# Kernel optimization log

Hardware: AMD Instinct MI355X
Metric: run time of the kernel (lower is better)

## Reference

```python
import jax, jax.numpy as jnp
import numpy as np
import math

D = 256; NH = 8; NL = 1; K = 5; P = K * K; HD = D // NH; DFF = 1024
N = 8192; H = 512; W = 512


def _kernel_indices():
    # odd kernel: linspace(-(K-1)/2, (K-1)/2, K) / K, meshgrid ij, stacked (x=j, y=i)
    idx = jnp.linspace(-(K - 1) / 2, (K - 1) / 2, K)
    i, j = jnp.meshgrid(idx, idx, indexing='ij')
    return jnp.stack([j, i], axis=-1).reshape(-1, 2) / K  # (P, 2)


def _ln(x, g, b, eps=1e-5):
    m = x.mean(-1, keepdims=True)
    v = ((x - m) ** 2).mean(-1, keepdims=True)
    return (x - m) / jnp.sqrt(v + eps) * g + b


def setup_inputs() -> dict:
    key = jax.random.key(0)
    ks = jax.random.split(key, 20)
    s = 0.02
    inp = {
        'query': jax.random.normal(ks[0], (1, N, D), jnp.float32),
        'memory': jax.random.normal(ks[1], (1, H * W, D), jnp.float32),
        'ref_windows': jax.random.uniform(ks[2], (1, N, 8), jnp.float32),
        'memory_shape': jnp.array([[H, W]], jnp.int32),
        'memory_start_idx': jnp.zeros((1,), jnp.int64),
        # pos embed MLP(8 -> D -> D -> D)
        'Wp1': jax.random.normal(ks[3], (D, 8)) * s, 'bp1': jnp.zeros((D,)),
        'Wp2': jax.random.normal(ks[4], (D, D)) * s, 'bp2': jnp.zeros((D,)),
        'Wp3': jax.random.normal(ks[5], (D, D)) * s, 'bp3': jnp.zeros((D,)),
        # Box3dAttention
        'Wv': jax.random.normal(ks[6], (D, D)) * s, 'bv': jnp.zeros((D,)),
        'Wa': jax.random.normal(ks[7], (NH * NL * P, D)) * s, 'ba': jnp.zeros((NH * NL * P,)),
        'Wb': jax.random.normal(ks[8], (NH * NL * 5, D)) * s, 'bb': jnp.zeros((NH * NL * 5,)),
        'Wo': jax.random.normal(ks[9], (D, D)) * s, 'bo': jnp.zeros((D,)),
        # FFN + norms
        'W1': jax.random.normal(ks[10], (DFF, D)) * s, 'b1': jnp.zeros((DFF,)),
        'W2': jax.random.normal(ks[11], (D, DFF)) * s, 'b2': jnp.zeros((D,)),
        'g2': jnp.ones((D,)), 'be2': jnp.zeros((D,)),
        'g3': jnp.ones((D,)), 'be3': jnp.zeros((D,)),
    }
    return inp


def reference(query, memory, ref_windows, memory_shape, memory_start_idx,
              Wp1, bp1, Wp2, bp2, Wp3, bp3, Wv, bv, Wa, ba, Wb, bb, Wo, bo,
              W1, b1, W2, b2, g2, be2, g3, be3):
    B, n, _ = query.shape  # B == 1, single level (NL == 1)
    # query positional embedding from ref windows (3-layer MLP)
    qp = jax.nn.relu(ref_windows @ Wp1.T + bp1)
    qp = jax.nn.relu(qp @ Wp2.T + bp2)
    qp = qp @ Wp3.T + bp3
    q = query + qp

    # --- Box3dAttention ---
    v = (memory @ Wv.T + bv).reshape(B, H * W, NH, HD)
    attn = jax.nn.softmax((q @ Wa.T + ba).reshape(B, n, NH, NL * P), axis=-1)
    attn = attn.reshape(B, n, NH, NL, P)

    off = (q @ Wb.T + bb).reshape(B, n, NH, NL, 5)
    off_box, off_ang = off[..., :4], off[..., 4:]
    rw = ref_windows[:, :, None, None]                     # (B,n,1,1,8)
    ref_boxes = rw[..., jnp.array([0, 1, 3, 4])]           # cx,cy,w,l
    ref_angle = rw[..., 6:7]
    angles = (ref_angle + off_ang / 16.0) * (2.0 * math.pi)  # (B,n,NH,NL,1)
    boxes = ref_boxes + off_box / 8.0 * ref_boxes[..., jnp.array([2, 3, 2, 3])]
    center = boxes[..., None, :2]                          # (B,n,NH,NL,1,2)
    size = jax.nn.relu(boxes[..., None, 2:])
    grid = _kernel_indices() * size                        # (B,n,NH,NL,P,2)
    c, sgn = jnp.cos(angles), jnp.sin(angles)
    rot = jnp.stack([c, -sgn, sgn, c], -1).reshape(B, n, NH, NL, 1, 2, 2)
    loc = center + (grid[..., None, :] * rot).sum(-1)      # (B,n,NH,NL,P,2) in [0,1]

    # bilinear sampling (grid_sample, align_corners=False, zero padding), single level
    loc0 = loc[0, :, :, 0]                                 # (n,NH,P,2)
    vh = v[0].transpose(1, 0, 2)                           # (NH,HW,HD)
    x = loc0[..., 0] * W - 0.5
    y = loc0[..., 1] * H - 0.5
    x0 = jnp.floor(x); y0 = jnp.floor(y)
    hidx = jnp.arange(NH)[None, :, None]
    out = jnp.zeros((n, NH, P, HD), v.dtype)
    for dx, dy in ((0, 0), (1, 0), (0, 1), (1, 1)):
        xi = x0 + dx; yi = y0 + dy
        wgt = (1.0 - jnp.abs(x - xi)) * (1.0 - jnp.abs(y - yi))
        valid = (xi >= 0) & (xi <= W - 1) & (yi >= 0) & (yi <= H - 1)
        idx = (jnp.clip(yi, 0, H - 1) * W + jnp.clip(xi, 0, W - 1)).astype(jnp.int32)
        g = vh[hidx, idx]                                  # (n,NH,P,HD)
        out = out + jnp.where(valid, wgt, 0.0)[..., None] * g
    out = (out * attn[0, :, :, 0, :, None]).sum(2)         # (n,NH,HD)
    q2 = out.reshape(1, n, D) @ Wo.T + bo

    # residual + LN + FFN + LN
    xq = _ln(query + q2, g2, be2)
    ff = jax.nn.relu(xq @ W1.T + b1) @ W2.T + b2
    return _ln(xq + ff, g3, be3)
```

## Files before the change

kernel.cpp:

```cpp
#include <hip/hip_runtime.h>
#include <hip/hip_bf16.h>
#include <math.h>

#define NQ 8192
#define DD 256
#define NHD 8
#define HDD 32
#define PP 25
#define HH 512
#define WW 512
#define HWSZ (HH * WW)
#define DFF 1024

typedef __bf16 bf16_t;
typedef bf16_t bf16x8 __attribute__((ext_vector_type(8)));
typedef bf16_t bf16x4 __attribute__((ext_vector_type(4)));
typedef float f32x4 __attribute__((ext_vector_type(4)));

template <int A_F32, int RELU, int ADD_RES, int BF16_OUT>
__global__ __launch_bounds__(256) void gemm_mfma(
    const void* __restrict__ Av, const bf16_t* __restrict__ Wt,
    const float* __restrict__ bias, const float* __restrict__ res,
    void* __restrict__ Cout, int M, int N, int K) {
  __shared__ bf16_t As[128][32];
  __shared__ bf16_t Bs[128][32];
  const int tid = threadIdx.x;
  const int bn = blockIdx.x * 128;
  const int bm = blockIdx.y * 128;
  const int wave = tid >> 6;
  const int lane = tid & 63;
  const int l15 = lane & 15;
  const int quad = lane >> 4;
  const int wm = (wave & 1) * 64;
  const int wn = (wave >> 1) * 64;

  f32x4 acc[4][4];
#pragma unroll
  for (int i = 0; i < 4; i++)
#pragma unroll
    for (int j = 0; j < 4; j++) acc[i][j] = (f32x4){0.f, 0.f, 0.f, 0.f};

  const int srow = tid >> 2;
  const int skq = (tid & 3) * 8;

  for (int k0 = 0; k0 < K; k0 += 32) {
    if (A_F32) {
      const float* A = (const float*)Av;
#pragma unroll
      for (int c = 0; c < 4; c++) {
        const int id = c * 256 + tid;
        const int row = id >> 3;
        const int kq = (id & 7) * 4;
        const float4 av = *(const float4*)(A + (long)(bm + row) * K + k0 + kq);
        bf16x4 bv;
        bv[0] = (bf16_t)av.x;
        bv[1] = (bf16_t)av.y;
        bv[2] = (bf16_t)av.z;
        bv[3] = (bf16_t)av.w;
        *(bf16x4*)&As[row][kq] = bv;
      }
    } else {
      const bf16_t* A = (const bf16_t*)Av;
#pragma unroll
      for (int c = 0; c < 2; c++) {
        const int row = c * 64 + srow;
        const bf16_t* gp = A + (long)(bm + row) * K + k0 + skq;
        bf16_t* lp = &As[0][0] + (c * 2048 + wave * 512);
        __builtin_amdgcn_global_load_lds(
            (const __attribute__((address_space(1))) void*)gp,
            (__attribute__((address_space(3))) void*)lp, 16, 0, 0);
      }
    }
#pragma unroll
    for (int c = 0; c < 2; c++) {
      const int row = c * 64 + srow;
      int wrow = bn + row;
      if (wrow >= N) wrow = N - 1;
      const bf16_t* gp = Wt + (long)wrow * K + k0 + skq;
      bf16_t* lp = &Bs[0][0] + (c * 2048 + wave * 512);
      __builtin_amdgcn_global_load_lds(
          (const __attribute__((address_space(1))) void*)gp,
          (__attribute__((address_space(3))) void*)lp, 16, 0, 0);
    }
    __syncthreads();
    bf16x8 af[4], bfr[4];
#pragma unroll
    for (int i = 0; i < 4; i++)
      af[i] = *(bf16x8*)&As[wm + i * 16 + l15][quad * 8];
#pragma unroll
    for (int j = 0; j < 4; j++)
      bfr[j] = *(bf16x8*)&Bs[wn + j * 16 + l15][quad * 8];
#pragma unroll
    for (int i = 0; i < 4; i++)
#pragma unroll
      for (int j = 0; j < 4; j++)
        acc[i][j] = __builtin_amdgcn_mfma_f32_16x16x32_bf16(af[i], bfr[j],
                                                            acc[i][j], 0, 0, 0);
    __syncthreads();
  }

  float bsv[4];
#pragma unroll
  for (int j = 0; j < 4; j++) {
    const int n = bn + wn + j * 16 + l15;
    bsv[j] = (n < N) ? bias[n] : 0.f;
  }
#pragma unroll
  for (int i = 0; i < 4; i++) {
#pragma unroll
    for (int r = 0; r < 4; r++) {
      const int m = bm + wm + i * 16 + quad * 4 + r;
#pragma unroll
      for (int j = 0; j < 4; j++) {
        const int n = bn + wn + j * 16 + l15;
        if (n < N) {
          float v = acc[i][j][r] + bsv[j];
          if (ADD_RES) v += res[(long)m * N + n];
          if (RELU) v = fmaxf(v, 0.f);
          if (BF16_OUT)
            ((__hip_bfloat16*)Cout)[(long)m * N + n] = __float2bfloat16(v);
          else
            ((float*)Cout)[(long)m * N + n] = v;
        }
      }
    }
  }
}

struct CastArgs {
  const float* src[8];
  __hip_bfloat16* dst[8];
  int len[8];
};
__global__ __launch_bounds__(256) void cast_weights(CastArgs a) {
  const int seg = blockIdx.y;
  const int base = blockIdx.x * 1024 + threadIdx.x * 4;
  if (base >= a.len[seg]) return;
  const float4 v = *(const float4*)(a.src[seg] + base);
  __hip_bfloat16* d = a.dst[seg] + base;
  d[0] = __float2bfloat16(v.x);
  d[1] = __float2bfloat16(v.y);
  d[2] = __float2bfloat16(v.z);
  d[3] = __float2bfloat16(v.w);
}

__global__ __launch_bounds__(256) void qp1_kernel(
    const float* __restrict__ rw, const float* __restrict__ Wp1,
    const float* __restrict__ bp1, __hip_bfloat16* __restrict__ out) {
  const int m = blockIdx.x;
  const int d = threadIdx.x;
  __shared__ float r[8];
  if (d < 8) r[d] = rw[m * 8 + d];
  __syncthreads();
  float s = bp1[d];
#pragma unroll
  for (int j = 0; j < 8; j++) s += r[j] * Wp1[d * 8 + j];
  out[(long)m * DD + d] = __float2bfloat16(fmaxf(s, 0.f));
}

__global__ __launch_bounds__(256) void attn_loc_kernel(
    const float* __restrict__ logits, const float* __restrict__ offp,
    const float* __restrict__ rw, float* __restrict__ attn,
    float* __restrict__ loc) {
  const int m = blockIdx.x;
  const int t = threadIdx.x;
  __shared__ float sl[200];
  __shared__ float soff[40];
  __shared__ float srw[8];
  if (t < 200) sl[t] = logits[(long)m * 200 + t];
  if (t >= 208 && t < 248) soff[t - 208] = offp[(long)m * 40 + (t - 208)];
  if (t >= 200 && t < 208) srw[t - 200] = rw[(long)m * 8 + (t - 200)];
  __syncthreads();
  if (t < 8) {
    float mx = -1e30f;
    for (int p = 0; p < 25; p++) mx = fmaxf(mx, sl[t * 25 + p]);
    float s = 0.f;
    for (int p = 0; p < 25; p++) s += __expf(sl[t * 25 + p] - mx);
    const float inv = 1.f / s;
    for (int p = 0; p < 25; p++)
      attn[(long)m * 200 + t * 25 + p] = __expf(sl[t * 25 + p] - mx) * inv;
  }
  if (t < 200) {
    const int h = t / 25;
    const int p = t - h * 25;
    const float cx = srw[0], cy = srw[1], w0 = srw[3], h0 = srw[4],
                ra = srw[6];
    const float ob0 = soff[h * 5 + 0], ob1 = soff[h * 5 + 1],
                ob2 = soff[h * 5 + 2], ob3 = soff[h * 5 + 3],
                oa = soff[h * 5 + 4];
    const float ang = (ra + oa * (1.f / 16.f)) * 6.28318530717958647692f;
    const float bx = cx + ob0 * 0.125f * w0;
    const float by = cy + ob1 * 0.125f * h0;
    const float bw = fmaxf(w0 + ob2 * 0.125f * w0, 0.f);
    const float bh = fmaxf(h0 + ob3 * 0.125f * h0, 0.f);
    const float gx = (float)((p % 5) - 2) * 0.2f * bw;
    const float gy = (float)((p / 5) - 2) * 0.2f * bh;
    float sn, cs;
    __sincosf(ang, &sn, &cs);
    loc[((long)m * 200 + t) * 2 + 0] = bx + cs * gx - sn * gy;
    loc[((long)m * 200 + t) * 2 + 1] = by + sn * gx + cs * gy;
  }
}

__global__ __launch_bounds__(256) void sample_kernel(
    const __hip_bfloat16* __restrict__ v, const float* __restrict__ attn,
    const float* __restrict__ loc, __hip_bfloat16* __restrict__ out) {
  const int m = blockIdx.x;
  const int t = threadIdx.x;
  const int h = t >> 5;
  const int c = t & 31;
  __shared__ float sat[200];
  __shared__ float slc[400];
  if (t < 200) sat[t] = attn[(long)m * 200 + t];
  slc[t] = loc[(long)m * 400 + t];
  if (t < 144) slc[256 + t] = loc[(long)m * 400 + 256 + t];
  __syncthreads();
  float acc = 0.f;
  for (int p = 0; p < 25; p++) {
    const float lx = slc[(h * 25 + p) * 2 + 0];
    const float ly = slc[(h * 25 + p) * 2 + 1];
    const float a = sat[h * 25 + p];
    const float x = lx * (float)WW - 0.5f;
    const float y = ly * (float)HH - 0.5f;
    const float x0 = floorf(x);
    const float y0 = floorf(y);
    float sval = 0.f;
#pragma unroll
    for (int dy = 0; dy < 2; dy++)
#pragma unroll
      for (int dx = 0; dx < 2; dx++) {
        const float xi = x0 + (float)dx;
        const float yi = y0 + (float)dy;
        const float wgt = (1.f - fabsf(x - xi)) * (1.f - fabsf(y - yi));
        const bool valid = (xi >= 0.f) && (xi <= (float)(WW - 1)) &&
                           (yi >= 0.f) && (yi <= (float)(HH - 1));
        const int xc = (int)fminf(fmaxf(xi, 0.f), (float)(WW - 1));
        const int yc = (int)fminf(fmaxf(yi, 0.f), (float)(HH - 1));
        const int idx = yc * WW + xc;
        const float g = __bfloat162float(v[(long)idx * DD + h * HDD + c]);
        sval += (valid ? wgt : 0.f) * g;
      }
    acc += a * sval;
  }
  out[(long)m * DD + t] = __float2bfloat16(acc);
}

__global__ __launch_bounds__(256) void ln_kernel(
    const float* __restrict__ x, const float* __restrict__ resid,
    const float* __restrict__ g, const float* __restrict__ b,
    float* __restrict__ out, __hip_bfloat16* __restrict__ out_bf) {
  const int m = blockIdx.x;
  const int d = threadIdx.x;
  const float v = x[(long)m * DD + d] + resid[(long)m * DD + d];
  __shared__ float red[256];
  __shared__ float mean_s, inv_s;
  red[d] = v;
  __syncthreads();
  for (int s = 128; s > 0; s >>= 1) {
    if (d < s) red[d] += red[d + s];
    __syncthreads();
  }
  if (d == 0) mean_s = red[0] * (1.f / 256.f);
  __syncthreads();
  const float mu = mean_s;
  const float diff = v - mu;
  red[d] = diff * diff;
  __syncthreads();
  for (int s = 128; s > 0; s >>= 1) {
    if (d < s) red[d] += red[d + s];
    __syncthreads();
  }
  if (d == 0) inv_s = rsqrtf(red[0] * (1.f / 256.f) + 1e-5f);
  __syncthreads();
  const float o = diff * inv_s * g[d] + b[d];
  out[(long)m * DD + d] = o;
  if (out_bf) out_bf[(long)m * DD + d] = __float2bfloat16(o);
}

extern "C" void kernel_launch(void* const* d_in, const int* in_sizes, int n_in,
                              void* d_out, int out_size, void* d_ws,
                              size_t ws_size, hipStream_t stream) {
  const float* query = (const float*)d_in[0];
  const float* memory = (const float*)d_in[1];
  const float* rw = (const float*)d_in[2];
  const float* Wp1 = (const float*)d_in[5];
  const float* bp1 = (const float*)d_in[6];
  const float* Wp2 = (const float*)d_in[7];
  const float* bp2 = (const float*)d_in[8];
  const float* Wp3 = (const float*)d_in[9];
  const float* bp3 = (const float*)d_in[10];
  const float* Wv = (const float*)d_in[11];
  const float* bv = (const float*)d_in[12];
  const float* Wa = (const float*)d_in[13];
  const float* ba = (const float*)d_in[14];
  const float* Wb = (const float*)d_in[15];
  const float* bb = (const float*)d_in[16];
  const float* Wo = (const float*)d_in[17];
  const float* bo = (const float*)d_in[18];
  const float* W1 = (const float*)d_in[19];
  const float* b1 = (const float*)d_in[20];
  const float* W2 = (const float*)d_in[21];
  const float* b2 = (const float*)d_in[22];
  const float* g2 = (const float*)d_in[23];
  const float* be2 = (const float*)d_in[24];
  const float* g3 = (const float*)d_in[25];
  const float* be3 = (const float*)d_in[26];

  char* ws = (char*)d_ws;
  size_t off = 0;
  auto alloc = [&](size_t bytes) {
    void* p = ws + off;
    off += (bytes + 255) & ~(size_t)255;
    return p;
  };
  __hip_bfloat16* vbuf = (__hip_bfloat16*)alloc((size_t)HWSZ * DD * 2);
  __hip_bfloat16* qp1bf = (__hip_bfloat16*)alloc((size_t)NQ * DD * 2);
  __hip_bfloat16* qp2bf = (__hip_bfloat16*)alloc((size_t)NQ * DD * 2);
  __hip_bfloat16* qbf = (__hip_bfloat16*)alloc((size_t)NQ * DD * 2);
  __hip_bfloat16* oabf = (__hip_bfloat16*)alloc((size_t)NQ * DD * 2);
  __hip_bfloat16* xqbf = (__hip_bfloat16*)alloc((size_t)NQ * DD * 2);
  __hip_bfloat16* h1bf = (__hip_bfloat16*)alloc((size_t)NQ * DFF * 2);
  float* xq32 = (float*)alloc((size_t)NQ * DD * 4);
  float* f32buf = (float*)alloc((size_t)NQ * DD * 4);
  float* offbuf = (float*)alloc((size_t)NQ * 40 * 4);
  float* attnbuf = (float*)alloc((size_t)NQ * 200 * 4);
  float* locbuf = (float*)alloc((size_t)NQ * 200 * 2 * 4);
  __hip_bfloat16* Wp2b = (__hip_bfloat16*)alloc(65536 * 2);
  __hip_bfloat16* Wp3b = (__hip_bfloat16*)alloc(65536 * 2);
  __hip_bfloat16* Wvb = (__hip_bfloat16*)alloc(65536 * 2);
  __hip_bfloat16* Wab = (__hip_bfloat16*)alloc(51200 * 2);
  __hip_bfloat16* Wbb = (__hip_bfloat16*)alloc(10240 * 2);
  __hip_bfloat16* Wob = (__hip_bfloat16*)alloc(65536 * 2);
  __hip_bfloat16* W1b = (__hip_bfloat16*)alloc(262144 * 2);
  __hip_bfloat16* W2b = (__hip_bfloat16*)alloc(262144 * 2);
  (void)ws_size;

  CastArgs ca;
  ca.src[0] = Wp2; ca.dst[0] = Wp2b; ca.len[0] = 65536;
  ca.src[1] = Wp3; ca.dst[1] = Wp3b; ca.len[1] = 65536;
  ca.src[2] = Wv;  ca.dst[2] = Wvb;  ca.len[2] = 65536;
  ca.src[3] = Wa;  ca.dst[3] = Wab;  ca.len[3] = 51200;
  ca.src[4] = Wb;  ca.dst[4] = Wbb;  ca.len[4] = 10240;
  ca.src[5] = Wo;  ca.dst[5] = Wob;  ca.len[5] = 65536;
  ca.src[6] = W1;  ca.dst[6] = W1b;  ca.len[6] = 262144;
  ca.src[7] = W2;  ca.dst[7] = W2b;  ca.len[7] = 262144;
  cast_weights<<<dim3(256, 8), 256, 0, stream>>>(ca);

  qp1_kernel<<<NQ, 256, 0, stream>>>(rw, Wp1, bp1, qp1bf);
  gemm_mfma<0, 1, 0, 1><<<dim3(2, NQ / 128), 256, 0, stream>>>(
      qp1bf, (const bf16_t*)Wp2b, bp2, nullptr, qp2bf, NQ, DD, DD);
  gemm_mfma<0, 0, 1, 1><<<dim3(2, NQ / 128), 256, 0, stream>>>(
      qp2bf, (const bf16_t*)Wp3b, bp3, query, qbf, NQ, DD, DD);
  gemm_mfma<1, 0, 0, 1><<<dim3(2, HWSZ / 128), 256, 0, stream>>>(
      memory, (const bf16_t*)Wvb, bv, nullptr, vbuf, HWSZ, DD, DD);
  gemm_mfma<0, 0, 0, 0><<<dim3(2, NQ / 128), 256, 0, stream>>>(
      qbf, (const bf16_t*)Wab, ba, nullptr, f32buf, NQ, 200, DD);
  gemm_mfma<0, 0, 0, 0><<<dim3(1, NQ / 128), 256, 0, stream>>>(
      qbf, (const bf16_t*)Wbb, bb, nullptr, offbuf, NQ, 40, DD);
  attn_loc_kernel<<<NQ, 256, 0, stream>>>(f32buf, offbuf, rw, attnbuf, locbuf);
  sample_kernel<<<NQ, 256, 0, stream>>>(vbuf, attnbuf, locbuf, oabf);
  gemm_mfma<0, 0, 0, 0><<<dim3(2, NQ / 128), 256, 0, stream>>>(
      oabf, (const bf16_t*)Wob, bo, nullptr, f32buf, NQ, DD, DD);
  ln_kernel<<<NQ, 256, 0, stream>>>(f32buf, query, g2, be2, xq32, xqbf);
  gemm_mfma<0, 1, 0, 1><<<dim3(8, NQ / 128), 256, 0, stream>>>(
      xqbf, (const bf16_t*)W1b, b1, nullptr, h1bf, NQ, DFF, DD);
  gemm_mfma<0, 0, 0, 0><<<dim3(2, NQ / 128), 256, 0, stream>>>(
      h1bf, (const bf16_t*)W2b, b2, nullptr, f32buf, NQ, DD, DFF);
  ln_kernel<<<NQ, 256, 0, stream>>>(f32buf, xq32, g3, be3, (float*)d_out,
                                    nullptr);
}
```

Baseline: 778.1 us.

## Add register-resident-weight value projection kernel and vectorize bilinear sampling taps

Replaces the generic LDS-tiled GEMM for the large memory value projection with a dedicated kernel. Each wave keeps its 64-column slice of Wv in registers and streams fp32 memory rows directly into MFMA fragments, so the weight is never reloaded through shared memory and the A tile skips the LDS round trip. The sampling kernel now assigns one bilinear tap and four channels to each thread, using 8-byte vector loads and cross-lane shuffles to combine the four taps. The trade-offs are higher register pressure in the new projection kernel and extra shuffles in the sampler.

```diff
diff --git a/kernel.cpp b/kernel.cpp
--- a/kernel.cpp
+++ b/kernel.cpp
@@ -17,9 +17,71 @@
 typedef bf16_t bf16x4 __attribute__((ext_vector_type(4)));
 typedef float f32x4 __attribute__((ext_vector_type(4)));
 
-template <int A_F32, int RELU, int ADD_RES, int BF16_OUT>
+__global__ __launch_bounds__(256, 2) void wv_kernel(
+    const float* __restrict__ A, const bf16_t* __restrict__ Wt,
+    const float* __restrict__ bias, __hip_bfloat16* __restrict__ V) {
+  const int tid = threadIdx.x;
+  const int wave = tid >> 6;
+  const int lane = tid & 63;
+  const int l15 = lane & 15;
+  const int quad = lane >> 4;
+  const int wslice = wave * 64;
+  const int base = blockIdx.x * 256;
+
+  bf16x8 bfr[4][8];
+#pragma unroll
+  for (int j = 0; j < 4; j++) {
+    const bf16_t* wp = Wt + (size_t)(wslice + j * 16 + l15) * 256 + quad * 8;
+#pragma unroll
+    for (int kt = 0; kt < 8; kt++) bfr[j][kt] = *(const bf16x8*)(wp + kt * 32);
+  }
+  float bsv[4];
+#pragma unroll
+  for (int j = 0; j < 4; j++) bsv[j] = bias[wslice + j * 16 + l15];
+
+  for (int c = 0; c < 16; c++) {
+    const int m0 = base + c * 16;
+    const float* ap = A + (size_t)(m0 + l15) * 256 + quad * 8;
+    float4 av[8][2];
+#pragma unroll
+    for (int kt = 0; kt < 8; kt++) {
+      av[kt][0] = *(const float4*)(ap + kt * 32);
+      av[kt][1] = *(const float4*)(ap + kt * 32 + 4);
+    }
+    f32x4 acc[4];
+#pragma unroll
+    for (int j = 0; j < 4; j++) acc[j] = (f32x4){0.f, 0.f, 0.f, 0.f};
+#pragma unroll
+    for (int kt = 0; kt < 8; kt++) {
+      bf16x8 afr;
+      afr[0] = (bf16_t)av[kt][0].x;
+      afr[1] = (bf16_t)av[kt][0].y;
+      afr[2] = (bf16_t)av[kt][0].z;
+      afr[3] = (bf16_t)av[kt][0].w;
+      afr[4] = (bf16_t)av[kt][1].x;
+      afr[5] = (bf16_t)av[kt][1].y;
+      afr[6] = (bf16_t)av[kt][1].z;
+      afr[7] = (bf16_t)av[kt][1].w;
+#pragma unroll
+      for (int j = 0; j < 4; j++)
+        acc[j] = __builtin_amdgcn_mfma_f32_16x16x32_bf16(afr, bfr[j][kt],
+                                                         acc[j], 0, 0, 0);
+    }
+#pragma unroll
+    for (int j = 0; j < 4; j++) {
+      const int col = wslice + j * 16 + l15;
+#pragma unroll
+      for (int r = 0; r < 4; r++) {
+        const int row = m0 + quad * 4 + r;
+        V[(size_t)row * DD + col] = __float2bfloat16(acc[j][r] + bsv[j]);
+      }
+    }
+  }
+}
+
+template <int RELU, int ADD_RES, int BF16_OUT>
 __global__ __launch_bounds__(256) void gemm_mfma(
-    const void* __restrict__ Av, const bf16_t* __restrict__ Wt,
+    const bf16_t* __restrict__ A, const bf16_t* __restrict__ Wt,
     const float* __restrict__ bias, const float* __restrict__ res,
     void* __restrict__ Cout, int M, int N, int K) {
   __shared__ bf16_t As[128][32];
@@ -44,32 +106,14 @@
   const int skq = (tid & 3) * 8;
 
   for (int k0 = 0; k0 < K; k0 += 32) {
-    if (A_F32) {
-      const float* A = (const float*)Av;
-#pragma unroll
-      for (int c = 0; c < 4; c++) {
-        const int id = c * 256 + tid;
-        const int row = id >> 3;
-        const int kq = (id & 7) * 4;
-        const float4 av = *(const float4*)(A + (long)(bm + row) * K + k0 + kq);
-        bf16x4 bv;
-        bv[0] = (bf16_t)av.x;
-        bv[1] = (bf16_t)av.y;
-        bv[2] = (bf16_t)av.z;
-        bv[3] = (bf16_t)av.w;
-        *(bf16x4*)&As[row][kq] = bv;
-      }
-    } else {
-      const bf16_t* A = (const bf16_t*)Av;
-#pragma unroll
-      for (int c = 0; c < 2; c++) {
-        const int row = c * 64 + srow;
-        const bf16_t* gp = A + (long)(bm + row) * K + k0 + skq;
-        bf16_t* lp = &As[0][0] + (c * 2048 + wave * 512);
-        __builtin_amdgcn_global_load_lds(
-            (const __attribute__((address_space(1))) void*)gp,
-            (__attribute__((address_space(3))) void*)lp, 16, 0, 0);
-      }
+#pragma unroll
+    for (int c = 0; c < 2; c++) {
+      const int row = c * 64 + srow;
+      const bf16_t* gp = A + (long)(bm + row) * K + k0 + skq;
+      bf16_t* lp = &As[0][0] + (c * 2048 + wave * 512);
+      __builtin_amdgcn_global_load_lds(
+          (const __attribute__((address_space(1))) void*)gp,
+          (__attribute__((address_space(3))) void*)lp, 16, 0, 0);
     }
 #pragma unroll
     for (int c = 0; c < 2; c++) {
@@ -203,46 +247,56 @@
 }
 
 __global__ __launch_bounds__(256) void sample_kernel(
-    const __hip_bfloat16* __restrict__ v, const float* __restrict__ attn,
-    const float* __restrict__ loc, __hip_bfloat16* __restrict__ out) {
+    const bf16_t* __restrict__ v, const float* __restrict__ attn,
+    const float* __restrict__ loc, bf16_t* __restrict__ out) {
   const int m = blockIdx.x;
   const int t = threadIdx.x;
   const int h = t >> 5;
-  const int c = t & 31;
+  const int sub = t & 31;
+  const int tap = sub >> 3;
+  const int ch4 = (sub & 7) * 4;
+  const float fdx = (float)(tap & 1);
+  const float fdy = (float)(tap >> 1);
   __shared__ float sat[200];
   __shared__ float slc[400];
   if (t < 200) sat[t] = attn[(long)m * 200 + t];
   slc[t] = loc[(long)m * 400 + t];
   if (t < 144) slc[256 + t] = loc[(long)m * 400 + 256 + t];
   __syncthreads();
-  float acc = 0.f;
+  float a0 = 0.f, a1 = 0.f, a2 = 0.f, a3 = 0.f;
+  const bf16_t* vb = v + h * HDD + ch4;
   for (int p = 0; p < 25; p++) {
     const float lx = slc[(h * 25 + p) * 2 + 0];
     const float ly = slc[(h * 25 + p) * 2 + 1];
-    const float a = sat[h * 25 + p];
+    const float aw = sat[h * 25 + p];
     const float x = lx * (float)WW - 0.5f;
     const float y = ly * (float)HH - 0.5f;
     const float x0 = floorf(x);
     const float y0 = floorf(y);
-    float sval = 0.f;
-#pragma unroll
-    for (int dy = 0; dy < 2; dy++)
-#pragma unroll
-      for (int dx = 0; dx < 2; dx++) {
-        const float xi = x0 + (float)dx;
-        const float yi = y0 + (float)dy;
-        const float wgt = (1.f - fabsf(x - xi)) * (1.f - fabsf(y - yi));
-        const bool valid = (xi >= 0.f) && (xi <= (float)(WW - 1)) &&
-                           (yi >= 0.f) && (yi <= (float)(HH - 1));
-        const int xc = (int)fminf(fmaxf(xi, 0.f), (float)(WW - 1));
-        const int yc = (int)fminf(fmaxf(yi, 0.f), (float)(HH - 1));
-        const int idx = yc * WW + xc;
-        const float g = __bfloat162float(v[(long)idx * DD + h * HDD + c]);
-        sval += (valid ? wgt : 0.f) * g;
-      }
-    acc += a * sval;
-  }
-  out[(long)m * DD + t] = __float2bfloat16(acc);
+    const float xi = x0 + fdx;
+    const float yi = y0 + fdy;
+    const float wgt = (1.f - fabsf(x - xi)) * (1.f - fabsf(y - yi));
+    const bool valid = (xi >= 0.f) && (xi <= (float)(WW - 1)) &&
+                       (yi >= 0.f) && (yi <= (float)(HH - 1));
+    const int xc = (int)fminf(fmaxf(xi, 0.f), (float)(WW - 1));
+    const int yc = (int)fminf(fmaxf(yi, 0.f), (float)(HH - 1));
+    const int idx = yc * WW + xc;
+    const bf16x4 g = *(const bf16x4*)(vb + (size_t)idx * DD);
+    const float wv = valid ? aw * wgt : 0.f;
+    a0 += wv * (float)g[0];
+    a1 += wv * (float)g[1];
+    a2 += wv * (float)g[2];
+    a3 += wv * (float)g[3];
+  }
+  a0 += __shfl_xor(a0, 8);  a1 += __shfl_xor(a1, 8);
+  a2 += __shfl_xor(a2, 8);  a3 += __shfl_xor(a3, 8);
+  a0 += __shfl_xor(a0, 16); a1 += __shfl_xor(a1, 16);
+  a2 += __shfl_xor(a2, 16); a3 += __shfl_xor(a3, 16);
+  if (tap == 0) {
+    bf16x4 o;
+    o[0] = (bf16_t)a0; o[1] = (bf16_t)a1; o[2] = (bf16_t)a2; o[3] = (bf16_t)a3;
+    *(bf16x4*)(out + (size_t)m * DD + h * HDD + ch4) = o;
+  }
 }
 
 __global__ __launch_bounds__(256) void ln_kernel(
@@ -347,25 +401,30 @@
   cast_weights<<<dim3(256, 8), 256, 0, stream>>>(ca);
 
   qp1_kernel<<<NQ, 256, 0, stream>>>(rw, Wp1, bp1, qp1bf);
-  gemm_mfma<0, 1, 0, 1><<<dim3(2, NQ / 128), 256, 0, stream>>>(
-      qp1bf, (const bf16_t*)Wp2b, bp2, nullptr, qp2bf, NQ, DD, DD);
-  gemm_mfma<0, 0, 1, 1><<<dim3(2, NQ / 128), 256, 0, stream>>>(
-      qp2bf, (const bf16_t*)Wp3b, bp3, query, qbf, NQ, DD, DD);
-  gemm_mfma<1, 0, 0, 1><<<dim3(2, HWSZ / 128), 256, 0, stream>>>(
-      memory, (const bf16_t*)Wvb, bv, nullptr, vbuf, HWSZ, DD, DD);
-  gemm_mfma<0, 0, 0, 0><<<dim3(2, NQ / 128), 256, 0, stream>>>(
-      qbf, (const bf16_t*)Wab, ba, nullptr, f32buf, NQ, 200, DD);
-  gemm_mfma<0, 0, 0, 0><<<dim3(1, NQ / 128), 256, 0, stream>>>(
-      qbf, (const bf16_t*)Wbb, bb, nullptr, offbuf, NQ, 40, DD);
+  gemm_mfma<1, 0, 1><<<dim3(2, NQ / 128), 256, 0, stream>>>(
+      (const bf16_t*)qp1bf, (const bf16_t*)Wp2b, bp2, nullptr, qp2bf, NQ, DD,
+      DD);
+  gemm_mfma<0, 1, 1><<<dim3(2, NQ / 128), 256, 0, stream>>>(
+      (const bf16_t*)qp2bf, (const bf16_t*)Wp3b, bp3, query, qbf, NQ, DD, DD);
+  wv_kernel<<<HWSZ / 256, 256, 0, stream>>>(memory, (const bf16_t*)Wvb, bv,
+                                            vbuf);
+  gemm_mfma<0, 0, 0><<<dim3(2, NQ / 128), 256, 0, stream>>>(
+      (const bf16_t*)qbf, (const bf16_t*)Wab, ba, nullptr, f32buf, NQ, 200,
+      DD);
+  gemm_mfma<0, 0, 0><<<dim3(1, NQ / 128), 256, 0, stream>>>(
+      (const bf16_t*)qbf, (const bf16_t*)Wbb, bb, nullptr, offbuf, NQ, 40, DD);
   attn_loc_kernel<<<NQ, 256, 0, stream>>>(f32buf, offbuf, rw, attnbuf, locbuf);
-  sample_kernel<<<NQ, 256, 0, stream>>>(vbuf, attnbuf, locbuf, oabf);
-  gemm_mfma<0, 0, 0, 0><<<dim3(2, NQ / 128), 256, 0, stream>>>(
-      oabf, (const bf16_t*)Wob, bo, nullptr, f32buf, NQ, DD, DD);
+  sample_kernel<<<NQ, 256, 0, stream>>>((const bf16_t*)vbuf, attnbuf, locbuf,
+                                        (bf16_t*)oabf);
+  gemm_mfma<0, 0, 0><<<dim3(2, NQ / 128), 256, 0, stream>>>(
+      (const bf16_t*)oabf, (const bf16_t*)Wob, bo, nullptr, f32buf, NQ, DD,
+      DD);
   ln_kernel<<<NQ, 256, 0, stream>>>(f32buf, query, g2, be2, xq32, xqbf);
-  gemm_mfma<0, 1, 0, 1><<<dim3(8, NQ / 128), 256, 0, stream>>>(
-      xqbf, (const bf16_t*)W1b, b1, nullptr, h1bf, NQ, DFF, DD);
-  gemm_mfma<0, 0, 0, 0><<<dim3(2, NQ / 128), 256, 0, stream>>>(
-      h1bf, (const bf16_t*)W2b, b2, nullptr, f32buf, NQ, DD, DFF);
+  gemm_mfma<1, 0, 1><<<dim3(8, NQ / 128), 256, 0, stream>>>(
+      (const bf16_t*)xqbf, (const bf16_t*)W1b, b1, nullptr, h1bf, NQ, DFF, DD);
+  gemm_mfma<0, 0, 0><<<dim3(2, NQ / 128), 256, 0, stream>>>(
+      (const bf16_t*)h1bf, (const bf16_t*)W2b, b2, nullptr, f32buf, NQ, DD,
+      DFF);
   ln_kernel<<<NQ, 256, 0, stream>>>(f32buf, xq32, g3, be3, (float*)d_out,
                                     nullptr);
 }
```

New measurement: 825.6 us. +6.1%, slower.
